# Kernel optimization log

Measured on AMD Instinct MI355X. Metric: run time of the kernel, lower is better.

The kernel has to match this reference:

```python
import jax, jax.numpy as jnp
import numpy as np

BETA = 0.5      # Tukey power transform exponent (args['beta'])
EPS = 1e-12     # F.normalize eps


def setup_inputs() -> dict:
    key = jax.random.key(0)
    k1, k2, k3 = jax.random.split(key, 3)
    B, C, D = 512, 200, 768
    raw_features = jax.random.normal(k1, (B, D), jnp.float32)
    class_means = jax.random.normal(k2, (C, D), jnp.float32)
    # Build SPD-like stacked inverse covariances [C, D, D] (as pinv of a
    # shrunk+normalized covariance would be symmetric PSD).
    A = jax.random.normal(k3, (C, D, D), jnp.float32) / jnp.sqrt(D)
    inv_covs = jnp.einsum('cij,ckj->cik', A, A) + 0.1 * jnp.eye(D, dtype=jnp.float32)
    return {
        'raw_features': raw_features,
        'class_means': class_means,
        'inv_covs': inv_covs,
        'active_classes': C,
    }


def reference(raw_features, class_means, inv_covs, active_classes):
    # Tukey transform: sign(x) * |x|^beta  (applied once, not per class)
    v = jnp.sign(raw_features) * jnp.abs(raw_features) ** BETA          # [B, D]
    # L2 normalize features (once) and class means
    v = v / jnp.clip(jnp.linalg.norm(v, axis=-1, keepdims=True), EPS)
    m = class_means / jnp.clip(
        jnp.linalg.norm(class_means, axis=-1, keepdims=True), EPS)      # [C, D]
    diff = v[:, None, :] - m[None, :, :]                                # [B, C, D]
    # Batched Mahalanobis quadratic form: all classes in one fused contraction
    left = jnp.einsum('bcd,cde->bce', diff, inv_covs)                   # [B, C, D]
    mahal = jnp.sum(left * diff, axis=-1)                               # [B, C]
    return -mahal
```

## Files before the change

kernel.cpp:

```cpp
#include <hip/hip_runtime.h>


#define B_SZ 512
#define C_SZ 200
#define D_SZ 768
#define BM 128
#define BN 128
#define BK 32
#define LDT 40
#define NK (D_SZ / BK)

typedef __bf16 bf16x8 __attribute__((ext_vector_type(8)));
typedef float  f32x4  __attribute__((ext_vector_type(4)));

__global__ __launch_bounds__(256)
void fecam_prep(const float* __restrict__ raw,
                const float* __restrict__ cmeans,
                float* __restrict__ v_out,
                float* __restrict__ m_out,
                float* __restrict__ out)
{
    const int blk = blockIdx.x;
    const int tid = threadIdx.x;
    if (blk >= B_SZ + C_SZ) {
        const int base = (blk - (B_SZ + C_SZ)) * 1024;
        #pragma unroll
        for (int i = 0; i < 4; ++i) {
            int idx = base + i * 256 + tid;
            if (idx < B_SZ * C_SZ) out[idx] = 0.0f;
        }
        return;
    }
    const bool is_feat = (blk < B_SZ);
    const float* src = is_feat ? (raw    + (size_t)blk          * D_SZ)
                               : (cmeans + (size_t)(blk - B_SZ) * D_SZ);
    float*       dst = is_feat ? (v_out  + (size_t)blk          * D_SZ)
                               : (m_out  + (size_t)(blk - B_SZ) * D_SZ);
    float vals[3];
    float ss = 0.0f;
    #pragma unroll
    for (int i = 0; i < 3; ++i) {
        float xx = src[tid + i * 256];
        if (is_feat) xx = copysignf(sqrtf(fabsf(xx)), xx);
        vals[i] = xx;
        ss += xx * xx;
    }
    #pragma unroll
    for (int off = 32; off; off >>= 1) ss += __shfl_xor(ss, off);
    __shared__ float red[4];
    if ((tid & 63) == 0) red[tid >> 6] = ss;
    __syncthreads();
    const float tot = red[0] + red[1] + red[2] + red[3];
    const float inv = 1.0f / fmaxf(sqrtf(tot), 1e-12f);
    #pragma unroll
    for (int i = 0; i < 3; ++i) dst[tid + i * 256] = vals[i] * inv;
}

__global__ __launch_bounds__(256, 2)
void fecam_mahal(const float* __restrict__ v,
                 const float* __restrict__ m,
                 const float* __restrict__ invc,
                 float* __restrict__ out)
{
    __shared__ __bf16 As[BM * LDT];
    __shared__ __bf16 Bs[BN * LDT];

    const int rr = blockIdx.x;
    const int x  = rr & 7;
    const int t  = rr >> 3;
    const int rb = t & 3;
    const int pg = t >> 2;
    const int p  = pg * 8 + x;
    const int c  = p / 6;
    const int dt = p - c * 6;
    const int b0 = rb * BM;
    const int d0 = dt * BN;

    const int tid = threadIdx.x;
    const int row = tid >> 1;
    const int eh  = (tid & 1) * 16;

    const float* vsrc = v    + (size_t)(b0 + row) * D_SZ + eh;
    const float* msrc = m    + (size_t)c * D_SZ + eh;
    const float* bsrc = invc + (size_t)c * D_SZ * D_SZ + (size_t)(d0 + row) * D_SZ + eh;

    const int lane = tid & 63;
    const int w    = tid >> 6;
    const int wr   = w >> 1;
    const int wc   = w & 1;
    const int l15  = lane & 15;
    const int g    = lane >> 4;

    f32x4 acc[4][4] = {};
    float4 va[4], vm[4], vb[4];

    #define LOADS(kk) do {                                                  \
        const int e0_ = (kk) * BK;                                          \
        _Pragma("unroll")                                                   \
        for (int i_ = 0; i_ < 4; ++i_) {                                    \
            va[i_] = *(const float4*)(vsrc + e0_ + i_ * 4);                 \
            vm[i_] = *(const float4*)(msrc + e0_ + i_ * 4);                 \
            vb[i_] = *(const float4*)(bsrc + e0_ + i_ * 4);                 \
        }                                                                   \
    } while (0)

    LOADS(0);

    for (int k = 0; k < NK; ++k) {
        if (k) __syncthreads();
        {
            float af[16], bq[16];
            #pragma unroll
            for (int i = 0; i < 4; ++i) {
                af[i*4+0] = va[i].x - vm[i].x;  af[i*4+1] = va[i].y - vm[i].y;
                af[i*4+2] = va[i].z - vm[i].z;  af[i*4+3] = va[i].w - vm[i].w;
                bq[i*4+0] = vb[i].x; bq[i*4+1] = vb[i].y;
                bq[i*4+2] = vb[i].z; bq[i*4+3] = vb[i].w;
            }
            bf16x8 pa0, pa1, pb0, pb1;
            #pragma unroll
            for (int i = 0; i < 8; ++i) {
                pa0[i] = (__bf16)af[i];   pa1[i] = (__bf16)af[8 + i];
                pb0[i] = (__bf16)bq[i];   pb1[i] = (__bf16)bq[8 + i];
            }
            *(bf16x8*)&As[row * LDT + eh]     = pa0;
            *(bf16x8*)&As[row * LDT + eh + 8] = pa1;
            *(bf16x8*)&Bs[row * LDT + eh]     = pb0;
            *(bf16x8*)&Bs[row * LDT + eh + 8] = pb1;
        }
        __syncthreads();
        if (k + 1 < NK) LOADS(k + 1);

        bf16x8 afr[4], bfr[4];
        #pragma unroll
        for (int mm = 0; mm < 4; ++mm)
            afr[mm] = *(const bf16x8*)&As[(wr*64 + mm*16 + l15) * LDT + g*8];
        #pragma unroll
        for (int nn = 0; nn < 4; ++nn)
            bfr[nn] = *(const bf16x8*)&Bs[(wc*64 + nn*16 + l15) * LDT + g*8];
        #pragma unroll
        for (int mm = 0; mm < 4; ++mm) {
            #pragma unroll
            for (int nn = 0; nn < 4; ++nn)
                acc[mm][nn] = __builtin_amdgcn_mfma_f32_16x16x32_bf16(
                    afr[mm], bfr[nn], acc[mm][nn], 0, 0, 0);
        }
    }
    #undef LOADS

    const int based = d0 + wc * 64 + l15;
    float md[4];
    #pragma unroll
    for (int nn = 0; nn < 4; ++nn) md[nn] = m[(size_t)c * D_SZ + based + nn * 16];
    #pragma unroll
    for (int mm = 0; mm < 4; ++mm) {
        #pragma unroll
        for (int j = 0; j < 4; ++j) {
            const int b = b0 + wr * 64 + mm * 16 + g * 4 + j;
            float s = 0.0f;
            #pragma unroll
            for (int nn = 0; nn < 4; ++nn) {
                const float dv = v[(size_t)b * D_SZ + based + nn * 16] - md[nn];
                s += acc[mm][nn][j] * dv;
            }
            s += __shfl_xor(s, 1);
            s += __shfl_xor(s, 2);
            s += __shfl_xor(s, 4);
            s += __shfl_xor(s, 8);
            if (l15 == 0) atomicAdd(&out[(size_t)b * C_SZ + c], -s);
        }
    }
}

extern "C" void kernel_launch(void* const* d_in, const int* in_sizes, int n_in,
                              void* d_out, int out_size, void* d_ws, size_t ws_size,
                              hipStream_t stream)
{
    const float* raw    = (const float*)d_in[0];
    const float* cmeans = (const float*)d_in[1];
    const float* invc   = (const float*)d_in[2];
    float* out = (float*)d_out;

    float* v  = (float*)d_ws;
    float* mn = v + (size_t)B_SZ * D_SZ;

    fecam_prep<<<B_SZ + C_SZ + 100, 256, 0, stream>>>(raw, cmeans, v, mn, out);
    fecam_mahal<<<(C_SZ * 6) * 4, 256, 0, stream>>>(v, mn, invc, out);
}
```

Measured before the change: 910.5 us.

## Expand Mahalanobis form to GEMM on shared bf16 features with async LDS loads

The quadratic form is expanded algebraically so the GEMM multiplies the class-independent normalized features v by the inverse covariance, instead of building (v - m) per class. The mean terms are folded in separately: m^T S m is accumulated from the B tile, and the epilogue uses (2m - v). The prep kernel now also writes v in a pre-tiled bf16 layout, which the main kernel streams straight into double-buffered LDS with global_load_lds. This removes the per-tile subtract and convert work and overlaps the A loads with the MFMAs. The cost is extra workspace and a larger LDS footprint, and cancellation in the expanded form can lose some precision.

```diff
diff --git a/kernel.cpp b/kernel.cpp
--- a/kernel.cpp
+++ b/kernel.cpp
@@ -4,21 +4,21 @@
 #define B_SZ 512
 #define C_SZ 200
 #define D_SZ 768
-#define BM 128
-#define BN 128
-#define BK 32
-#define LDT 40
-#define NK (D_SZ / BK)
+#define NK   24
 
 typedef __bf16 bf16x8 __attribute__((ext_vector_type(8)));
 typedef float  f32x4  __attribute__((ext_vector_type(4)));
 
+__device__ __forceinline__ void gl16(const __bf16* g, __bf16* l) {
+    __builtin_amdgcn_global_load_lds(
+        (const __attribute__((address_space(1))) void*)g,
+        (__attribute__((address_space(3))) void*)l, 16, 0, 0);
+}
+
 __global__ __launch_bounds__(256)
-void fecam_prep(const float* __restrict__ raw,
-                const float* __restrict__ cmeans,
-                float* __restrict__ v_out,
-                float* __restrict__ m_out,
-                float* __restrict__ out)
+void fecam_prep(const float* __restrict__ raw, const float* __restrict__ cmeans,
+                float* __restrict__ v_out, float* __restrict__ m_out,
+                __bf16* __restrict__ vt, float* __restrict__ out)
 {
     const int blk = blockIdx.x;
     const int tid = threadIdx.x;
@@ -31,143 +31,165 @@
         }
         return;
     }
-    const bool is_feat = (blk < B_SZ);
-    const float* src = is_feat ? (raw    + (size_t)blk          * D_SZ)
-                               : (cmeans + (size_t)(blk - B_SZ) * D_SZ);
-    float*       dst = is_feat ? (v_out  + (size_t)blk          * D_SZ)
-                               : (m_out  + (size_t)(blk - B_SZ) * D_SZ);
-    float vals[3];
-    float ss = 0.0f;
+    const bool isf = (blk < B_SZ);
+    const float* src = isf ? raw + (size_t)blk * D_SZ
+                           : cmeans + (size_t)(blk - B_SZ) * D_SZ;
+    float vals[3]; float ss = 0.f;
     #pragma unroll
     for (int i = 0; i < 3; ++i) {
         float xx = src[tid + i * 256];
-        if (is_feat) xx = copysignf(sqrtf(fabsf(xx)), xx);
-        vals[i] = xx;
-        ss += xx * xx;
+        if (isf) xx = copysignf(sqrtf(fabsf(xx)), xx);
+        vals[i] = xx; ss += xx * xx;
     }
     #pragma unroll
     for (int off = 32; off; off >>= 1) ss += __shfl_xor(ss, off);
     __shared__ float red[4];
     if ((tid & 63) == 0) red[tid >> 6] = ss;
     __syncthreads();
-    const float tot = red[0] + red[1] + red[2] + red[3];
-    const float inv = 1.0f / fmaxf(sqrtf(tot), 1e-12f);
-    #pragma unroll
-    for (int i = 0; i < 3; ++i) dst[tid + i * 256] = vals[i] * inv;
+    const float inv = 1.0f / fmaxf(sqrtf(red[0] + red[1] + red[2] + red[3]), 1e-12f);
+    if (isf) {
+        const int b = blk;
+        #pragma unroll
+        for (int i = 0; i < 3; ++i) {
+            const int e = tid + i * 256;
+            const float val = vals[i] * inv;
+            v_out[(size_t)b * D_SZ + e] = val;
+            const int idx = ((b >> 7) * NK + (e >> 5)) * 4096
+                          + ((e >> 3) & 3) * 1024 + (b & 127) * 8 + (e & 7);
+            vt[idx] = (__bf16)val;
+        }
+    } else {
+        float* dst = m_out + (size_t)(blk - B_SZ) * D_SZ;
+        #pragma unroll
+        for (int i = 0; i < 3; ++i) dst[tid + i * 256] = vals[i] * inv;
+    }
 }
 
 __global__ __launch_bounds__(256, 2)
-void fecam_mahal(const float* __restrict__ v,
-                 const float* __restrict__ m,
-                 const float* __restrict__ invc,
+void fecam_mahal(const float* __restrict__ v, const float* __restrict__ m,
+                 const __bf16* __restrict__ vt, const float* __restrict__ invc,
                  float* __restrict__ out)
 {
-    __shared__ __bf16 As[BM * LDT];
-    __shared__ __bf16 Bs[BN * LDT];
+    __shared__ __bf16 As[2][4096];
+    __shared__ __bf16 Bs[2][4096];
+    __shared__ float  ms[D_SZ];
+    __shared__ float  reds[4];
 
     const int rr = blockIdx.x;
-    const int x  = rr & 7;
-    const int t  = rr >> 3;
-    const int rb = t & 3;
-    const int pg = t >> 2;
+    const int x  = rr & 7, tt = rr >> 3;
+    const int rb = tt & 3, pg = tt >> 2;
     const int p  = pg * 8 + x;
-    const int c  = p / 6;
-    const int dt = p - c * 6;
-    const int b0 = rb * BM;
-    const int d0 = dt * BN;
+    const int c  = p / 6, dt = p - c * 6;
+    const int b0 = rb * 128, d0 = dt * 128;
 
     const int tid = threadIdx.x;
-    const int row = tid >> 1;
-    const int eh  = (tid & 1) * 16;
-
-    const float* vsrc = v    + (size_t)(b0 + row) * D_SZ + eh;
-    const float* msrc = m    + (size_t)c * D_SZ + eh;
-    const float* bsrc = invc + (size_t)c * D_SZ * D_SZ + (size_t)(d0 + row) * D_SZ + eh;
-
-    const int lane = tid & 63;
-    const int w    = tid >> 6;
-    const int wr   = w >> 1;
-    const int wc   = w & 1;
-    const int l15  = lane & 15;
-    const int g    = lane >> 4;
-
-    f32x4 acc[4][4] = {};
-    float4 va[4], vm[4], vb[4];
-
-    #define LOADS(kk) do {                                                  \
-        const int e0_ = (kk) * BK;                                          \
-        _Pragma("unroll")                                                   \
-        for (int i_ = 0; i_ < 4; ++i_) {                                    \
-            va[i_] = *(const float4*)(vsrc + e0_ + i_ * 4);                 \
-            vm[i_] = *(const float4*)(msrc + e0_ + i_ * 4);                 \
-            vb[i_] = *(const float4*)(bsrc + e0_ + i_ * 4);                 \
-        }                                                                   \
-    } while (0)
-
-    LOADS(0);
-
-    for (int k = 0; k < NK; ++k) {
-        if (k) __syncthreads();
-        {
-            float af[16], bq[16];
-            #pragma unroll
-            for (int i = 0; i < 4; ++i) {
-                af[i*4+0] = va[i].x - vm[i].x;  af[i*4+1] = va[i].y - vm[i].y;
-                af[i*4+2] = va[i].z - vm[i].z;  af[i*4+3] = va[i].w - vm[i].w;
-                bq[i*4+0] = vb[i].x; bq[i*4+1] = vb[i].y;
-                bq[i*4+2] = vb[i].z; bq[i*4+3] = vb[i].w;
-            }
-            bf16x8 pa0, pa1, pb0, pb1;
-            #pragma unroll
-            for (int i = 0; i < 8; ++i) {
-                pa0[i] = (__bf16)af[i];   pa1[i] = (__bf16)af[8 + i];
-                pb0[i] = (__bf16)bq[i];   pb1[i] = (__bf16)bq[8 + i];
-            }
-            *(bf16x8*)&As[row * LDT + eh]     = pa0;
-            *(bf16x8*)&As[row * LDT + eh + 8] = pa1;
-            *(bf16x8*)&Bs[row * LDT + eh]     = pb0;
-            *(bf16x8*)&Bs[row * LDT + eh + 8] = pb1;
-        }
-        __syncthreads();
-        if (k + 1 < NK) LOADS(k + 1);
-
+    const int lane = tid & 63, w = tid >> 6;
+    const int wr = w >> 1, wc = w & 1;
+    const int l15 = lane & 15, g = lane >> 4;
+    const int drow = tid >> 1, eh = tid & 1;
+
+    const float*  bsrc  = invc + (size_t)c * D_SZ * D_SZ + (size_t)(d0 + drow) * D_SZ + eh * 16;
+    const __bf16* atile = vt + (size_t)rb * NK * 4096 + tid * 8;
+    const float*  mrow  = m + (size_t)c * D_SZ;
+
+    ms[tid]       = mrow[tid];
+    ms[tid + 256] = mrow[tid + 256];
+    ms[tid + 512] = mrow[tid + 512];
+
+    float4 vb[4];
+    float  sacc = 0.f;
+    f32x4  acc[4][4] = {};
+
+    auto issueB = [&](int kk) {
+        const float* s = bsrc + kk * 32;
+        vb[0] = *(const float4*)(s);
+        vb[1] = *(const float4*)(s + 4);
+        vb[2] = *(const float4*)(s + 8);
+        vb[3] = *(const float4*)(s + 12);
+    };
+    auto gloadA = [&](int kk, int buf) {
+        const __bf16* s = atile + kk * 4096;
+        gl16(s,        &As[buf][tid * 8]);
+        gl16(s + 2048, &As[buf][tid * 8 + 2048]);
+    };
+    auto writeB = [&](int buf, int kk) {
+        float f[16];
+        #pragma unroll
+        for (int i = 0; i < 4; ++i) {
+            f[i*4+0] = vb[i].x; f[i*4+1] = vb[i].y;
+            f[i*4+2] = vb[i].z; f[i*4+3] = vb[i].w;
+        }
+        const float* mse = &ms[kk * 32 + eh * 16];
+        float sl = 0.f;
+        #pragma unroll
+        for (int i = 0; i < 16; ++i) sl += f[i] * mse[i];
+        sacc += sl;
+        bf16x8 p0, p1;
+        #pragma unroll
+        for (int i = 0; i < 8; ++i) { p0[i] = (__bf16)f[i]; p1[i] = (__bf16)f[8+i]; }
+        *(bf16x8*)&Bs[buf][(eh*2 + 0) * 1024 + drow * 8] = p0;
+        *(bf16x8*)&Bs[buf][(eh*2 + 1) * 1024 + drow * 8] = p1;
+    };
+    auto mfmaPhase = [&](int buf) {
         bf16x8 afr[4], bfr[4];
         #pragma unroll
         for (int mm = 0; mm < 4; ++mm)
-            afr[mm] = *(const bf16x8*)&As[(wr*64 + mm*16 + l15) * LDT + g*8];
+            afr[mm] = *(const bf16x8*)&As[buf][g * 1024 + (wr*64 + mm*16 + l15) * 8];
         #pragma unroll
         for (int nn = 0; nn < 4; ++nn)
-            bfr[nn] = *(const bf16x8*)&Bs[(wc*64 + nn*16 + l15) * LDT + g*8];
-        #pragma unroll
-        for (int mm = 0; mm < 4; ++mm) {
+            bfr[nn] = *(const bf16x8*)&Bs[buf][g * 1024 + (wc*64 + nn*16 + l15) * 8];
+        #pragma unroll
+        for (int mm = 0; mm < 4; ++mm)
             #pragma unroll
             for (int nn = 0; nn < 4; ++nn)
                 acc[mm][nn] = __builtin_amdgcn_mfma_f32_16x16x32_bf16(
                     afr[mm], bfr[nn], acc[mm][nn], 0, 0, 0);
-        }
-    }
-    #undef LOADS
-
-    const int based = d0 + wc * 64 + l15;
-    float md[4];
-    #pragma unroll
-    for (int nn = 0; nn < 4; ++nn) md[nn] = m[(size_t)c * D_SZ + based + nn * 16];
+    };
+
+    issueB(0);
+    gloadA(0, 0);
+    __syncthreads();
+    writeB(0, 0);
+    __syncthreads();
+    issueB(1);
+
+    int cur = 0;
+    for (int k = 0; k < NK; ++k) {
+        if (k + 1 < NK) gloadA(k + 1, cur ^ 1);
+        mfmaPhase(cur);
+        if (k + 1 < NK) writeB(cur ^ 1, k + 1);
+        if (k + 1 < NK) __syncthreads();
+        if (k + 2 < NK) issueB(k + 2);
+        cur ^= 1;
+    }
+
+    float sthr = ms[d0 + drow] * sacc;
+    #pragma unroll
+    for (int off = 1; off < 64; off <<= 1) sthr += __shfl_xor(sthr, off);
+    if (lane == 0) reds[w] = sthr;
+    __syncthreads();
+    const float s_part = reds[0] + reds[1] + reds[2] + reds[3];
+
+    const int dbase = d0 + wc * 64 + l15;
+    float md2[4];
+    #pragma unroll
+    for (int nn = 0; nn < 4; ++nn) md2[nn] = 2.0f * ms[dbase - d0 + d0 + nn * 16];
     #pragma unroll
     for (int mm = 0; mm < 4; ++mm) {
         #pragma unroll
         for (int j = 0; j < 4; ++j) {
             const int b = b0 + wr * 64 + mm * 16 + g * 4 + j;
-            float s = 0.0f;
+            const float* vrow = v + (size_t)b * D_SZ + dbase;
+            float val = 0.f;
             #pragma unroll
-            for (int nn = 0; nn < 4; ++nn) {
-                const float dv = v[(size_t)b * D_SZ + based + nn * 16] - md[nn];
-                s += acc[mm][nn][j] * dv;
-            }
-            s += __shfl_xor(s, 1);
-            s += __shfl_xor(s, 2);
-            s += __shfl_xor(s, 4);
-            s += __shfl_xor(s, 8);
-            if (l15 == 0) atomicAdd(&out[(size_t)b * C_SZ + c], -s);
+            for (int nn = 0; nn < 4; ++nn)
+                val += acc[mm][nn][j] * (md2[nn] - vrow[nn * 16]);
+            val += __shfl_xor(val, 1);
+            val += __shfl_xor(val, 2);
+            val += __shfl_xor(val, 4);
+            val += __shfl_xor(val, 8);
+            if (l15 == 0)
+                atomicAdd(&out[(size_t)b * C_SZ + c], (wc == 0) ? (val - s_part) : val);
         }
     }
 }
@@ -181,9 +203,10 @@
     const float* invc   = (const float*)d_in[2];
     float* out = (float*)d_out;
 
-    float* v  = (float*)d_ws;
-    float* mn = v + (size_t)B_SZ * D_SZ;
-
-    fecam_prep<<<B_SZ + C_SZ + 100, 256, 0, stream>>>(raw, cmeans, v, mn, out);
-    fecam_mahal<<<(C_SZ * 6) * 4, 256, 0, stream>>>(v, mn, invc, out);
-}
+    float*  v  = (float*)d_ws;
+    float*  mn = v + (size_t)B_SZ * D_SZ;
+    __bf16* vt = (__bf16*)(mn + (size_t)C_SZ * D_SZ);
+
+    fecam_prep<<<B_SZ + C_SZ + 100, 256, 0, stream>>>(raw, cmeans, v, mn, vt, out);
+    fecam_mahal<<<4800, 256, 0, stream>>>(v, mn, vt, invc, out);
+}
```

Result: faster. 876.3 us (-3.8%).
